# Optimization experiments

Hardware: AMD Instinct MI355X
Metric: run time of the kernel (lower is better)

Reference implementation:

```python
import jax, jax.numpy as jnp
import numpy as np
import math

H = 8
D_MODEL = 512
D_K = D_MODEL // H
NEG = -1.0e9


def setup_inputs() -> dict:
    key = jax.random.key(0)
    ks = jax.random.split(key, 10)
    B, S, D = 8, 1024, D_MODEL
    s = 1.0 / math.sqrt(D)
    return {
        "query": jax.random.normal(ks[0], (B, S, D), jnp.float32),
        "key": jax.random.normal(ks[1], (B, S, D), jnp.float32),
        "value": jax.random.normal(ks[2], (B, S, D), jnp.float32),
        "group_prob": jax.random.uniform(ks[3], (B, S, S), jnp.float32),
        "Wq": jax.random.normal(ks[4], (D, D), jnp.float32) * s,
        "Wk": jax.random.normal(ks[5], (D, D), jnp.float32) * s,
        "Wv": jax.random.normal(ks[6], (D, D), jnp.float32) * s,
        "Wh": jax.random.normal(ks[7], (D, D), jnp.float32) * s,
        "bh": jax.random.normal(ks[8], (D,), jnp.float32) * s,
        "mask": jax.random.randint(ks[9], (B, S, S), 0, 2, jnp.int32),
    }


def reference(query, key, value, group_prob, Wq, Wk, Wv, Wh, bh, mask):
    B, S, D = query.shape
    # project and split heads: [B, H, S, d_k]
    def split(x, W):
        return (x @ W.T).reshape(B, S, H, D_K).transpose(0, 2, 1, 3)
    q, k, v = split(query, Wq), split(key, Wk), split(value, Wv)
    scores = jnp.einsum('bhqd,bhkd->bhqk', q, k) / jnp.sqrt(jnp.asarray(D_K, q.dtype))
    # masked_fill where (mask | eye) == 0, i.e. keep mask-allowed or diagonal positions
    eye = jnp.eye(S, dtype=jnp.int32)
    allowed = (mask[:, None, :, :] | eye[None, None, :, :]) != 0  # [B,1,S,S]
    scores = jnp.where(allowed, scores, jnp.asarray(NEG, scores.dtype))
    p_attn = jax.nn.softmax(scores, axis=-1)
    p_attn = p_attn * group_prob[:, None, :, :]  # post-softmax group scaling
    x = jnp.einsum('bhqk,bhkd->bhqd', p_attn, v)
    x = x.transpose(0, 2, 1, 3).reshape(B, S, D)
    return x @ Wh.T + bh
```

## Files before the change

### kernel.cpp

```cpp
#include <hip/hip_runtime.h>
#include <hip/hip_bf16.h>
#include <cstdint>


typedef __attribute__((ext_vector_type(8))) short short8;
typedef __attribute__((ext_vector_type(4))) float f32x4;

__device__ __forceinline__ ushort f2bf(float x) {
    union { __hip_bfloat16 h; ushort u; } v;
    v.h = __float2bfloat16(x);
    return v.u;
}
__device__ __forceinline__ float bf2f(ushort u) {
    union { uint u; float f; } v; v.u = ((uint)u) << 16; return v.f;
}
__device__ __forceinline__ uint cvtpk(float lo, float hi) {
    uint r;
    asm("v_cvt_pk_bf16_f32 %0, %1, %2" : "=v"(r) : "v"(lo), "v"(hi));
    return r;
}
__device__ __forceinline__ f32x4 mfma16(short8 a, short8 b, f32x4 c) {
    return __builtin_amdgcn_mfma_f32_16x16x32_bf16(a, b, c, 0, 0, 0);
}
__device__ __forceinline__ void gl16(const void* g, const void* l) {
    __builtin_amdgcn_global_load_lds(
        (const __attribute__((address_space(1))) uint32_t*)(uintptr_t)g,
        (__attribute__((address_space(3))) uint32_t*)(uint32_t)(uintptr_t)l,
        16, 0, 0);
}

__global__ __launch_bounds__(256)
void prep(const float* __restrict__ q, const float* __restrict__ k,
          const float* __restrict__ v,
          const float* __restrict__ wq, const float* __restrict__ wk,
          const float* __restrict__ wv, const float* __restrict__ wh,
          const int* __restrict__ mask, const float* __restrict__ gp,
          ushort* __restrict__ qb, ushort* __restrict__ kb,
          ushort* __restrict__ vb,
          ushort* __restrict__ wqb, ushort* __restrict__ wkb,
          ushort* __restrict__ wvb, ushort* __restrict__ whb,
          ushort* __restrict__ gmb)
{
    const int bid = blockIdx.x, tid = threadIdx.x;
    if (bid < 8192) {
        size_t i = ((size_t)bid * 256 + tid) * 4;
        int4 m = *(const int4*)(mask + i);
        float4 gg = *(const float4*)(gp + i);
        int kk = (int)(i & 1023), qq = (int)((i >> 10) & 1023);
        uint u01 = cvtpk(gg.x, gg.y), u23 = cvtpk(gg.z, gg.w);
        ushort4 o;
        o.x = (m.x != 0 || qq == kk + 0) ? (ushort)(u01 & 0xffff) : (ushort)0xBF80;
        o.y = (m.y != 0 || qq == kk + 1) ? (ushort)(u01 >> 16)    : (ushort)0xBF80;
        o.z = (m.z != 0 || qq == kk + 2) ? (ushort)(u23 & 0xffff) : (ushort)0xBF80;
        o.w = (m.w != 0 || qq == kk + 3) ? (ushort)(u23 >> 16)    : (ushort)0xBF80;
        *(ushort4*)(gmb + i) = o;
    } else if (bid < 20480) {
        size_t id = ((size_t)(bid - 8192) * 256 + tid) * 4;
        int t = (int)(id >> 22);
        size_t off = id & 4194303;
        const float* s = (t == 0) ? q : (t == 1) ? k : v;
        ushort* d = (t == 0) ? qb : (t == 1) ? kb : vb;
        float4 x = *(const float4*)(s + off);
        uint2 o; o.x = cvtpk(x.x, x.y); o.y = cvtpk(x.z, x.w);
        *(uint2*)(d + off) = o;
    } else {
        size_t id = ((size_t)(bid - 20480) * 256 + tid) * 4;
        int t = (int)(id >> 18);
        size_t off = id & 262143;
        const float* s = (t == 0) ? wq : (t == 1) ? wk : (t == 2) ? wv : wh;
        ushort* d = (t == 0) ? wqb : (t == 1) ? wkb : (t == 2) ? wvb : whb;
        float4 x = *(const float4*)(s + off);
        uint2 o; o.x = cvtpk(x.x, x.y); o.y = cvtpk(x.z, x.w);
        *(uint2*)(d + off) = o;
    }
}

__global__ __launch_bounds__(256, 2)
void gemm3(const ushort* __restrict__ qb, const ushort* __restrict__ kb,
           const ushort* __restrict__ vb,
           const ushort* __restrict__ Wqb, const ushort* __restrict__ Wkb,
           const ushort* __restrict__ Wvb,
           ushort* __restrict__ q_ws, ushort* __restrict__ k_ws,
           ushort* __restrict__ vT)
{
    __shared__ __attribute__((aligned(16))) ushort As[8192];
    __shared__ __attribute__((aligned(16))) ushort Bs[8192];

    const int z = blockIdx.z;
    const ushort* A = (z == 0) ? qb : (z == 1) ? kb : Wvb;
    const ushort* B = (z == 0) ? Wqb : (z == 1) ? Wkb : vb;
    const int mt = (z == 2) ? blockIdx.y : blockIdx.x;
    const int nt = (z == 2) ? blockIdx.x : blockIdx.y;
    const int m0 = mt * 128, n0 = nt * 128;
    const int tid = threadIdx.x, lane = tid & 63, wave = tid >> 6;
    const int l15 = lane & 15, g = lane >> 4;
    const int wm = wave >> 1, wn = wave & 1;

    const int cb = (lane & 7) << 4;
    int soff[4];
    #pragma unroll
    for (int it = 0; it < 4; ++it) {
        int r = (it * 4 + wave) * 8 + (lane >> 3);
        soff[it] = r * 1024 + (cb ^ ((r & 7) << 4));
    }
    const char* Ab = (const char*)A + (size_t)m0 * 1024;
    const char* Bb = (const char*)B + (size_t)n0 * 1024;

    const int sw = (l15 & 7) << 4;
    const int c0 = (g * 16) ^ sw;
    const int c1 = (64 + g * 16) ^ sw;

    f32x4 acc[4][4];
    #pragma unroll
    for (int i = 0; i < 4; ++i)
        #pragma unroll
        for (int j = 0; j < 4; ++j) acc[i][j] = (f32x4){0.f, 0.f, 0.f, 0.f};

    for (int ks = 0; ks < 8; ++ks) {
        const int kof = ks * 128;
        #pragma unroll
        for (int it = 0; it < 4; ++it) {
            gl16(Ab + soff[it] + kof, (const char*)As + (it * 4 + wave) * 1024);
            gl16(Bb + soff[it] + kof, (const char*)Bs + (it * 4 + wave) * 1024);
        }
        __syncthreads();
        #pragma unroll
        for (int kk = 0; kk < 2; ++kk) {
            const int cc = kk ? c1 : c0;
            short8 af[4], bf[4];
            #pragma unroll
            for (int i = 0; i < 4; ++i)
                af[i] = *(const short8*)((const char*)As + (wm * 64 + i * 16 + l15) * 128 + cc);
            #pragma unroll
            for (int j = 0; j < 4; ++j)
                bf[j] = *(const short8*)((const char*)Bs + (wn * 64 + j * 16 + l15) * 128 + cc);
            #pragma unroll
            for (int i = 0; i < 4; ++i)
                #pragma unroll
                for (int j = 0; j < 4; ++j)
                    acc[i][j] = mfma16(af[i], bf[j], acc[i][j]);
        }
        __syncthreads();
    }

    #pragma unroll
    for (int i = 0; i < 4; ++i) {
        #pragma unroll
        for (int j = 0; j < 4; ++j) {
            #pragma unroll
            for (int r = 0; r < 4; ++r) {
                int mm = m0 + wm * 64 + i * 16 + g * 4 + r;
                int nn = n0 + wn * 64 + j * 16 + l15;
                float val = acc[i][j][r];
                if (z == 0) {
                    val *= 0.18033688f;
                    int b = mm >> 10, s = mm & 1023, h = nn >> 6, dk = nn & 63;
                    q_ws[((((size_t)(b * 8 + h)) << 10) + s) * 64 + dk] = f2bf(val);
                } else if (z == 1) {
                    int b = mm >> 10, s = mm & 1023, h = nn >> 6, dk = nn & 63;
                    k_ws[((((size_t)(b * 8 + h)) << 10) + s) * 64 + dk] = f2bf(val);
                } else {
                    int h = mm >> 6, d = mm & 63, b = nn >> 10, s = nn & 1023;
                    vT[(((size_t)(b * 8 + h) * 64 + d) << 10) + s] = f2bf(val);
                }
            }
        }
    }
}

__global__ __launch_bounds__(256, 2)
void gemm_o(const ushort* __restrict__ Xh, const ushort* __restrict__ Whb,
            const float* __restrict__ bias, float* __restrict__ out)
{
    __shared__ __attribute__((aligned(16))) ushort As[8192];
    __shared__ __attribute__((aligned(16))) ushort Bs[8192];

    const int m0 = blockIdx.x * 128, n0 = blockIdx.y * 128;
    const int tid = threadIdx.x, lane = tid & 63, wave = tid >> 6;
    const int l15 = lane & 15, g = lane >> 4;
    const int wm = wave >> 1, wn = wave & 1;
    const int bb = m0 >> 10, s0 = m0 & 1023;

    const int cb = (lane & 7) << 4;
    int aoff[4], boff[4];
    #pragma unroll
    for (int it = 0; it < 4; ++it) {
        int r = (it * 4 + wave) * 8 + (lane >> 3);
        int swz = cb ^ ((r & 7) << 4);
        aoff[it] = ((bb * 8) * 1024 + s0 + r) * 128 + swz;
        boff[it] = (n0 + r) * 1024 + swz;
    }
    const int sw = (l15 & 7) << 4;
    const int c0 = (g * 16) ^ sw;
    const int c1 = (64 + g * 16) ^ sw;

    f32x4 acc[4][4];
    #pragma unroll
    for (int i = 0; i < 4; ++i)
        #pragma unroll
        for (int j = 0; j < 4; ++j) acc[i][j] = (f32x4){0.f, 0.f, 0.f, 0.f};

    for (int ks = 0; ks < 8; ++ks) {
        #pragma unroll
        for (int it = 0; it < 4; ++it) {
            gl16((const char*)Xh + aoff[it] + ks * 131072,
                 (const char*)As + (it * 4 + wave) * 1024);
            gl16((const char*)Whb + boff[it] + ks * 128,
                 (const char*)Bs + (it * 4 + wave) * 1024);
        }
        __syncthreads();
        #pragma unroll
        for (int kk = 0; kk < 2; ++kk) {
            const int cc = kk ? c1 : c0;
            short8 af[4], bf[4];
            #pragma unroll
            for (int i = 0; i < 4; ++i)
                af[i] = *(const short8*)((const char*)As + (wm * 64 + i * 16 + l15) * 128 + cc);
            #pragma unroll
            for (int j = 0; j < 4; ++j)
                bf[j] = *(const short8*)((const char*)Bs + (wn * 64 + j * 16 + l15) * 128 + cc);
            #pragma unroll
            for (int i = 0; i < 4; ++i)
                #pragma unroll
                for (int j = 0; j < 4; ++j)
                    acc[i][j] = mfma16(af[i], bf[j], acc[i][j]);
        }
        __syncthreads();
    }

    float bv[4];
    #pragma unroll
    for (int j = 0; j < 4; ++j) bv[j] = bias[n0 + wn * 64 + j * 16 + l15];

    #pragma unroll
    for (int i = 0; i < 4; ++i)
        #pragma unroll
        for (int j = 0; j < 4; ++j)
            #pragma unroll
            for (int r = 0; r < 4; ++r) {
                int mm = m0 + wm * 64 + i * 16 + g * 4 + r;
                int nn = n0 + wn * 64 + j * 16 + l15;
                out[(size_t)mm * 512 + nn] = acc[i][j][r] + bv[j];
            }
}

__global__ __launch_bounds__(256, 4)
void attn(const ushort* __restrict__ Qh, const ushort* __restrict__ Kh,
          const ushort* __restrict__ Vt, const ushort* __restrict__ gm,
          ushort* __restrict__ xo)
{
    __shared__ __attribute__((aligned(16))) ushort kv[2][2][4096];

    const int w = blockIdx.x;
    const int bh = w & 63, qt = w >> 6;
    const int tid = threadIdx.x, wave = tid >> 6, lane = tid & 63;
    const int l15 = lane & 15, g = lane >> 4;
    const int q0 = qt * 64 + wave * 16;
    const int b = bh >> 3;

    const char* Kpb = (const char*)(Kh + (size_t)bh * 65536);
    const char* Vpb = (const char*)(Vt + (size_t)bh * 65536);
    const ushort* Qp = Qh + ((size_t)bh * 1024 + q0 + l15) * 64;
    const ushort* gmp = gm + ((size_t)b * 1024 + q0 + l15) * 1024;

    const short8 qf0 = *(const short8*)(Qp + g * 8);
    const short8 qf1 = *(const short8*)(Qp + 32 + g * 8);

    const int cb = (lane & 7) << 4;
    const int rA = wave * 8 + (lane >> 3);
    const int rB = rA + 32;
    const int gkA = (rA & 3) + 4 * ((rA >> 4) & 1) + 8 * ((rA >> 2) & 3) + 32 * (rA >> 5);
    const int gkB = (rB & 3) + 4 * ((rB >> 4) & 1) + 8 * ((rB >> 2) & 3) + 32 * (rB >> 5);
    const int okA = gkA * 128 + (cb ^ ((rA & 7) << 4));
    const int okB = gkB * 128 + (cb ^ ((rB & 7) << 4));
    const int ovA = rA * 2048 + (cb ^ ((rA & 7) << 4));
    const int ovB = rB * 2048 + (cb ^ ((rB & 7) << 4));

    const int sw = (l15 & 7) << 4;
    const int c0 = (g * 16) ^ sw;
    const int c1 = (64 + g * 16) ^ sw;

    f32x4 ot[4];
    #pragma unroll
    for (int t = 0; t < 4; ++t) ot[t] = (f32x4){0.f, 0.f, 0.f, 0.f};
    float m2 = -1.0e30f, lsum = 0.f;

    gl16(Kpb + okA, &kv[0][0][wave * 512]);
    gl16(Kpb + okB, &kv[0][0][(4 + wave) * 512]);
    gl16(Vpb + ovA, &kv[0][1][wave * 512]);
    gl16(Vpb + ovB, &kv[0][1][(4 + wave) * 512]);
    short8 gmc0 = *(const short8*)(gmp + g * 8);
    short8 gmc1 = *(const short8*)(gmp + 32 + g * 8);
    __syncthreads();

    for (int t = 0; t < 16; ++t) {
        const int cur = t & 1;
        short8 gmn0, gmn1;
        if (t < 15) {
            const char* kp = Kpb + (size_t)(t + 1) * 8192;
            const char* vp = Vpb + (size_t)(t + 1) * 128;
            gl16(kp + okA, &kv[cur ^ 1][0][wave * 512]);
            gl16(kp + okB, &kv[cur ^ 1][0][(4 + wave) * 512]);
            gl16(vp + ovA, &kv[cur ^ 1][1][wave * 512]);
            gl16(vp + ovB, &kv[cur ^ 1][1][(4 + wave) * 512]);
            gmn0 = *(const short8*)(gmp + (t + 1) * 64 + g * 8);
            gmn1 = *(const short8*)(gmp + (t + 1) * 64 + 32 + g * 8);
        }
        const char* kbuf = (const char*)&kv[cur][0][0];
        const char* vbuf = (const char*)&kv[cur][1][0];

        f32x4 s4[4];
        #pragma unroll
        for (int t4 = 0; t4 < 4; ++t4) {
            const char* ka = kbuf + (t4 * 16 + l15) * 128;
            short8 k0f = *(const short8*)(ka + c0);
            short8 k1f = *(const short8*)(ka + c1);
            f32x4 zz = (f32x4){0.f, 0.f, 0.f, 0.f};
            zz = mfma16(k0f, qf0, zz);
            zz = mfma16(k1f, qf1, zz);
            s4[t4] = zz;
        }

        float gv[16], svv[16];
        #pragma unroll
        for (int c = 0; c < 2; ++c) {
            const short8 gc = c ? gmc1 : gmc0;
            #pragma unroll
            for (int j = 0; j < 8; ++j) {
                const int jj = c * 8 + j;
                const int t4 = 2 * c + (j >> 2), r = j & 3;
                float gvv = bf2f((ushort)gc[j]);
                gv[jj] = gvv;
                svv[jj] = (gvv >= 0.f) ? s4[t4][r] : -1.0e9f;
            }
        }
        float x0 = fmaxf(fmaxf(svv[0], svv[1]), fmaxf(svv[2], svv[3]));
        float x1 = fmaxf(fmaxf(svv[4], svv[5]), fmaxf(svv[6], svv[7]));
        float x2 = fmaxf(fmaxf(svv[8], svv[9]), fmaxf(svv[10], svv[11]));
        float x3 = fmaxf(fmaxf(svv[12], svv[13]), fmaxf(svv[14], svv[15]));
        float tmax = fmaxf(fmaxf(x0, x1), fmaxf(x2, x3));
        tmax = fmaxf(tmax, __shfl_xor(tmax, 16, 64));
        tmax = fmaxf(tmax, __shfl_xor(tmax, 32, 64));

        if (__any(tmax > m2 + 4.0f)) {
            float mnew = fmaxf(m2, tmax);
            float corr = exp2f(m2 - mnew);
            m2 = mnew; lsum *= corr;
            #pragma unroll
            for (int t4 = 0; t4 < 4; ++t4) {
                ot[t4][0] *= corr; ot[t4][1] *= corr;
                ot[t4][2] *= corr; ot[t4][3] *= corr;
            }
        }

        float p[16];
        #pragma unroll
        for (int jj = 0; jj < 16; ++jj) p[jj] = exp2f(svv[jj] - m2);
        lsum += (((p[0] + p[1]) + (p[2] + p[3])) + ((p[4] + p[5]) + (p[6] + p[7])))
              + (((p[8] + p[9]) + (p[10] + p[11])) + ((p[12] + p[13]) + (p[14] + p[15])));
        union { uint4 u; short8 s; } pa0, pa1;
        pa0.u.x = cvtpk(p[0] * gv[0],  p[1] * gv[1]);
        pa0.u.y = cvtpk(p[2] * gv[2],  p[3] * gv[3]);
        pa0.u.z = cvtpk(p[4] * gv[4],  p[5] * gv[5]);
        pa0.u.w = cvtpk(p[6] * gv[6],  p[7] * gv[7]);
        pa1.u.x = cvtpk(p[8] * gv[8],  p[9] * gv[9]);
        pa1.u.y = cvtpk(p[10] * gv[10], p[11] * gv[11]);
        pa1.u.z = cvtpk(p[12] * gv[12], p[13] * gv[13]);
        pa1.u.w = cvtpk(p[14] * gv[14], p[15] * gv[15]);

        #pragma unroll
        for (int td = 0; td < 4; ++td) {
            const char* va = vbuf + (td * 16 + l15) * 128;
            short8 v0 = *(const short8*)(va + c0);
            short8 v1 = *(const short8*)(va + c1);
            ot[td] = mfma16(v0, pa0.s, ot[td]);
            ot[td] = mfma16(v1, pa1.s, ot[td]);
        }
        __syncthreads();
        if (t < 15) { gmc0 = gmn0; gmc1 = gmn1; }
    }

    lsum += __shfl_xor(lsum, 16, 64);
    lsum += __shfl_xor(lsum, 32, 64);
    const float inv = 1.0f / lsum;

    ushort* xp = xo + ((size_t)bh * 1024 + q0 + l15) * 64;
    #pragma unroll
    for (int td = 0; td < 4; ++td) {
        uint2 o;
        o.x = cvtpk(ot[td][0] * inv, ot[td][1] * inv);
        o.y = cvtpk(ot[td][2] * inv, ot[td][3] * inv);
        *(uint2*)(xp + td * 16 + g * 4) = o;
    }
}

extern "C" void kernel_launch(void* const* d_in, const int* in_sizes, int n_in,
                              void* d_out, int out_size, void* d_ws, size_t ws_size,
                              hipStream_t stream)
{
    const float* query = (const float*)d_in[0];
    const float* key   = (const float*)d_in[1];
    const float* value = (const float*)d_in[2];
    const float* gprob = (const float*)d_in[3];
    const float* Wq    = (const float*)d_in[4];
    const float* Wk    = (const float*)d_in[5];
    const float* Wv    = (const float*)d_in[6];
    const float* Wh    = (const float*)d_in[7];
    const float* bh    = (const float*)d_in[8];
    const int*   mask  = (const int*)d_in[9];
    float* out = (float*)d_out;

    ushort* ws = (ushort*)d_ws;
    const size_t HS = (size_t)64 * 65536;
    ushort* q_ws = ws;
    ushort* k_ws = ws + HS;
    ushort* vT   = ws + 2 * HS;
    ushort* gmb  = ws + 3 * HS;
    ushort* qb   = ws + 5 * HS;
    ushort* kb   = ws + 6 * HS;
    ushort* vb   = ws + 7 * HS;
    ushort* wqb  = ws + 8 * HS;
    ushort* wkb  = wqb + 262144;
    ushort* wvb  = wkb + 262144;
    ushort* whb  = wvb + 262144;
    ushort* x_ws = qb;

    prep<<<21504, 256, 0, stream>>>(query, key, value, Wq, Wk, Wv, Wh,
                                    mask, gprob, qb, kb, vb,
                                    wqb, wkb, wvb, whb, gmb);
    gemm3<<<dim3(64, 4, 3), 256, 0, stream>>>(qb, kb, vb, wqb, wkb, wvb,
                                              q_ws, k_ws, vT);
    attn<<<1024, 256, 0, stream>>>(q_ws, k_ws, vT, gmb, x_ws);
    gemm_o<<<dim3(64, 4), 256, 0, stream>>>(x_ws, whb, bh, out);
}
```

Measured before the change: 102.3 us.

## Process two query tiles per wave and drop online softmax max tracking

Each wave in the attention kernel now handles 32 query rows as two 16-row tiles. Every K/V fragment read from LDS feeds twice as many MFMAs, and the block count drops to 512. The running-max rescaling in the softmax is removed: exponentials are taken directly on the raw scores and normalised at the end, which removes the cross-lane max reduction and the rescale branch. In exchange it doubles accumulator and score registers (launch bounds relaxed to 2 blocks per SIMD group), halves the grid, and risks overflow if scores ever become large.

```diff
diff --git a/kernel.cpp b/kernel.cpp
--- a/kernel.cpp
+++ b/kernel.cpp
@@ -244,7 +244,7 @@
             }
 }
 
-__global__ __launch_bounds__(256, 4)
+__global__ __launch_bounds__(256, 2)
 void attn(const ushort* __restrict__ Qh, const ushort* __restrict__ Kh,
           const ushort* __restrict__ Vt, const ushort* __restrict__ gm,
           ushort* __restrict__ xo)
@@ -255,16 +255,20 @@
     const int bh = w & 63, qt = w >> 6;
     const int tid = threadIdx.x, wave = tid >> 6, lane = tid & 63;
     const int l15 = lane & 15, g = lane >> 4;
-    const int q0 = qt * 64 + wave * 16;
+    const int q0 = qt * 128 + wave * 32;
     const int b = bh >> 3;
 
     const char* Kpb = (const char*)(Kh + (size_t)bh * 65536);
     const char* Vpb = (const char*)(Vt + (size_t)bh * 65536);
-    const ushort* Qp = Qh + ((size_t)bh * 1024 + q0 + l15) * 64;
-    const ushort* gmp = gm + ((size_t)b * 1024 + q0 + l15) * 1024;
-
-    const short8 qf0 = *(const short8*)(Qp + g * 8);
-    const short8 qf1 = *(const short8*)(Qp + 32 + g * 8);
+    const ushort* QpA = Qh + ((size_t)bh * 1024 + q0 + l15) * 64;
+    const ushort* QpB = QpA + 16 * 64;
+    const ushort* gmpA = gm + ((size_t)b * 1024 + q0 + l15) * 1024;
+    const ushort* gmpB = gmpA + 16 * 1024;
+
+    const short8 qa0 = *(const short8*)(QpA + g * 8);
+    const short8 qa1 = *(const short8*)(QpA + 32 + g * 8);
+    const short8 qb0 = *(const short8*)(QpB + g * 8);
+    const short8 qb1 = *(const short8*)(QpB + 32 + g * 8);
 
     const int cb = (lane & 7) << 4;
     const int rA = wave * 8 + (lane >> 3);
@@ -280,22 +284,27 @@
     const int c0 = (g * 16) ^ sw;
     const int c1 = (64 + g * 16) ^ sw;
 
-    f32x4 ot[4];
-    #pragma unroll
-    for (int t = 0; t < 4; ++t) ot[t] = (f32x4){0.f, 0.f, 0.f, 0.f};
-    float m2 = -1.0e30f, lsum = 0.f;
+    f32x4 otA[4], otB[4];
+    #pragma unroll
+    for (int t = 0; t < 4; ++t) {
+        otA[t] = (f32x4){0.f, 0.f, 0.f, 0.f};
+        otB[t] = (f32x4){0.f, 0.f, 0.f, 0.f};
+    }
+    float lsA = 0.f, lsB = 0.f;
 
     gl16(Kpb + okA, &kv[0][0][wave * 512]);
     gl16(Kpb + okB, &kv[0][0][(4 + wave) * 512]);
     gl16(Vpb + ovA, &kv[0][1][wave * 512]);
     gl16(Vpb + ovB, &kv[0][1][(4 + wave) * 512]);
-    short8 gmc0 = *(const short8*)(gmp + g * 8);
-    short8 gmc1 = *(const short8*)(gmp + 32 + g * 8);
+    short8 gcA0 = *(const short8*)(gmpA + g * 8);
+    short8 gcA1 = *(const short8*)(gmpA + 32 + g * 8);
+    short8 gcB0 = *(const short8*)(gmpB + g * 8);
+    short8 gcB1 = *(const short8*)(gmpB + 32 + g * 8);
     __syncthreads();
 
     for (int t = 0; t < 16; ++t) {
         const int cur = t & 1;
-        short8 gmn0, gmn1;
+        short8 gnA0, gnA1, gnB0, gnB1;
         if (t < 15) {
             const char* kp = Kpb + (size_t)(t + 1) * 8192;
             const char* vp = Vpb + (size_t)(t + 1) * 128;
@@ -303,94 +312,114 @@
             gl16(kp + okB, &kv[cur ^ 1][0][(4 + wave) * 512]);
             gl16(vp + ovA, &kv[cur ^ 1][1][wave * 512]);
             gl16(vp + ovB, &kv[cur ^ 1][1][(4 + wave) * 512]);
-            gmn0 = *(const short8*)(gmp + (t + 1) * 64 + g * 8);
-            gmn1 = *(const short8*)(gmp + (t + 1) * 64 + 32 + g * 8);
+            gnA0 = *(const short8*)(gmpA + (t + 1) * 64 + g * 8);
+            gnA1 = *(const short8*)(gmpA + (t + 1) * 64 + 32 + g * 8);
+            gnB0 = *(const short8*)(gmpB + (t + 1) * 64 + g * 8);
+            gnB1 = *(const short8*)(gmpB + (t + 1) * 64 + 32 + g * 8);
         }
         const char* kbuf = (const char*)&kv[cur][0][0];
         const char* vbuf = (const char*)&kv[cur][1][0];
 
-        f32x4 s4[4];
+        f32x4 sA[4], sB[4];
         #pragma unroll
         for (int t4 = 0; t4 < 4; ++t4) {
             const char* ka = kbuf + (t4 * 16 + l15) * 128;
             short8 k0f = *(const short8*)(ka + c0);
             short8 k1f = *(const short8*)(ka + c1);
-            f32x4 zz = (f32x4){0.f, 0.f, 0.f, 0.f};
-            zz = mfma16(k0f, qf0, zz);
-            zz = mfma16(k1f, qf1, zz);
-            s4[t4] = zz;
-        }
-
-        float gv[16], svv[16];
-        #pragma unroll
-        for (int c = 0; c < 2; ++c) {
-            const short8 gc = c ? gmc1 : gmc0;
-            #pragma unroll
-            for (int j = 0; j < 8; ++j) {
-                const int jj = c * 8 + j;
-                const int t4 = 2 * c + (j >> 2), r = j & 3;
-                float gvv = bf2f((ushort)gc[j]);
-                gv[jj] = gvv;
-                svv[jj] = (gvv >= 0.f) ? s4[t4][r] : -1.0e9f;
+            f32x4 za = (f32x4){0.f, 0.f, 0.f, 0.f};
+            za = mfma16(k0f, qa0, za);
+            za = mfma16(k1f, qa1, za);
+            sA[t4] = za;
+            f32x4 zb = (f32x4){0.f, 0.f, 0.f, 0.f};
+            zb = mfma16(k0f, qb0, zb);
+            zb = mfma16(k1f, qb1, zb);
+            sB[t4] = zb;
+        }
+
+        union { uint4 u; short8 s; } paA0, paA1, paB0, paB1;
+        {
+            float p[16], gv[16];
+            #pragma unroll
+            for (int c = 0; c < 2; ++c) {
+                const short8 gc = c ? gcA1 : gcA0;
+                #pragma unroll
+                for (int j = 0; j < 8; ++j) {
+                    const int jj = c * 8 + j;
+                    const int t4 = 2 * c + (j >> 2), r = j & 3;
+                    float gvv = bf2f((ushort)gc[j]);
+                    gv[jj] = gvv;
+                    p[jj] = exp2f((gvv >= 0.f) ? sA[t4][r] : -1.0e9f);
+                }
             }
-        }
-        float x0 = fmaxf(fmaxf(svv[0], svv[1]), fmaxf(svv[2], svv[3]));
-        float x1 = fmaxf(fmaxf(svv[4], svv[5]), fmaxf(svv[6], svv[7]));
-        float x2 = fmaxf(fmaxf(svv[8], svv[9]), fmaxf(svv[10], svv[11]));
-        float x3 = fmaxf(fmaxf(svv[12], svv[13]), fmaxf(svv[14], svv[15]));
-        float tmax = fmaxf(fmaxf(x0, x1), fmaxf(x2, x3));
-        tmax = fmaxf(tmax, __shfl_xor(tmax, 16, 64));
-        tmax = fmaxf(tmax, __shfl_xor(tmax, 32, 64));
-
-        if (__any(tmax > m2 + 4.0f)) {
-            float mnew = fmaxf(m2, tmax);
-            float corr = exp2f(m2 - mnew);
-            m2 = mnew; lsum *= corr;
-            #pragma unroll
-            for (int t4 = 0; t4 < 4; ++t4) {
-                ot[t4][0] *= corr; ot[t4][1] *= corr;
-                ot[t4][2] *= corr; ot[t4][3] *= corr;
+            lsA += (((p[0] + p[1]) + (p[2] + p[3])) + ((p[4] + p[5]) + (p[6] + p[7])))
+                 + (((p[8] + p[9]) + (p[10] + p[11])) + ((p[12] + p[13]) + (p[14] + p[15])));
+            paA0.u.x = cvtpk(p[0] * gv[0],  p[1] * gv[1]);
+            paA0.u.y = cvtpk(p[2] * gv[2],  p[3] * gv[3]);
+            paA0.u.z = cvtpk(p[4] * gv[4],  p[5] * gv[5]);
+            paA0.u.w = cvtpk(p[6] * gv[6],  p[7] * gv[7]);
+            paA1.u.x = cvtpk(p[8] * gv[8],  p[9] * gv[9]);
+            paA1.u.y = cvtpk(p[10] * gv[10], p[11] * gv[11]);
+            paA1.u.z = cvtpk(p[12] * gv[12], p[13] * gv[13]);
+            paA1.u.w = cvtpk(p[14] * gv[14], p[15] * gv[15]);
+        }
+        {
+            float p[16], gv[16];
+            #pragma unroll
+            for (int c = 0; c < 2; ++c) {
+                const short8 gc = c ? gcB1 : gcB0;
+                #pragma unroll
+                for (int j = 0; j < 8; ++j) {
+                    const int jj = c * 8 + j;
+                    const int t4 = 2 * c + (j >> 2), r = j & 3;
+                    float gvv = bf2f((ushort)gc[j]);
+                    gv[jj] = gvv;
+                    p[jj] = exp2f((gvv >= 0.f) ? sB[t4][r] : -1.0e9f);
+                }
             }
-        }
-
-        float p[16];
-        #pragma unroll
-        for (int jj = 0; jj < 16; ++jj) p[jj] = exp2f(svv[jj] - m2);
-        lsum += (((p[0] + p[1]) + (p[2] + p[3])) + ((p[4] + p[5]) + (p[6] + p[7])))
-              + (((p[8] + p[9]) + (p[10] + p[11])) + ((p[12] + p[13]) + (p[14] + p[15])));
-        union { uint4 u; short8 s; } pa0, pa1;
-        pa0.u.x = cvtpk(p[0] * gv[0],  p[1] * gv[1]);
-        pa0.u.y = cvtpk(p[2] * gv[2],  p[3] * gv[3]);
-        pa0.u.z = cvtpk(p[4] * gv[4],  p[5] * gv[5]);
-        pa0.u.w = cvtpk(p[6] * gv[6],  p[7] * gv[7]);
-        pa1.u.x = cvtpk(p[8] * gv[8],  p[9] * gv[9]);
-        pa1.u.y = cvtpk(p[10] * gv[10], p[11] * gv[11]);
-        pa1.u.z = cvtpk(p[12] * gv[12], p[13] * gv[13]);
-        pa1.u.w = cvtpk(p[14] * gv[14], p[15] * gv[15]);
+            lsB += (((p[0] + p[1]) + (p[2] + p[3])) + ((p[4] + p[5]) + (p[6] + p[7])))
+                 + (((p[8] + p[9]) + (p[10] + p[11])) + ((p[12] + p[13]) + (p[14] + p[15])));
+            paB0.u.x = cvtpk(p[0] * gv[0],  p[1] * gv[1]);
+            paB0.u.y = cvtpk(p[2] * gv[2],  p[3] * gv[3]);
+            paB0.u.z = cvtpk(p[4] * gv[4],  p[5] * gv[5]);
+            paB0.u.w = cvtpk(p[6] * gv[6],  p[7] * gv[7]);
+            paB1.u.x = cvtpk(p[8] * gv[8],  p[9] * gv[9]);
+            paB1.u.y = cvtpk(p[10] * gv[10], p[11] * gv[11]);
+            paB1.u.z = cvtpk(p[12] * gv[12], p[13] * gv[13]);
+            paB1.u.w = cvtpk(p[14] * gv[14], p[15] * gv[15]);
+        }
 
         #pragma unroll
         for (int td = 0; td < 4; ++td) {
             const char* va = vbuf + (td * 16 + l15) * 128;
             short8 v0 = *(const short8*)(va + c0);
             short8 v1 = *(const short8*)(va + c1);
-            ot[td] = mfma16(v0, pa0.s, ot[td]);
-            ot[td] = mfma16(v1, pa1.s, ot[td]);
+            otA[td] = mfma16(v0, paA0.s, otA[td]);
+            otA[td] = mfma16(v1, paA1.s, otA[td]);
+            otB[td] = mfma16(v0, paB0.s, otB[td]);
+            otB[td] = mfma16(v1, paB1.s, otB[td]);
         }
         __syncthreads();
-        if (t < 15) { gmc0 = gmn0; gmc1 = gmn1; }
-    }
-
-    lsum += __shfl_xor(lsum, 16, 64);
-    lsum += __shfl_xor(lsum, 32, 64);
-    const float inv = 1.0f / lsum;
-
-    ushort* xp = xo + ((size_t)bh * 1024 + q0 + l15) * 64;
+        if (t < 15) { gcA0 = gnA0; gcA1 = gnA1; gcB0 = gnB0; gcB1 = gnB1; }
+    }
+
+    lsA += __shfl_xor(lsA, 16, 64);
+    lsA += __shfl_xor(lsA, 32, 64);
+    lsB += __shfl_xor(lsB, 16, 64);
+    lsB += __shfl_xor(lsB, 32, 64);
+    const float invA = 1.0f / lsA;
+    const float invB = 1.0f / lsB;
+
+    ushort* xpA = xo + ((size_t)bh * 1024 + q0 + l15) * 64;
+    ushort* xpB = xpA + 16 * 64;
     #pragma unroll
     for (int td = 0; td < 4; ++td) {
-        uint2 o;
-        o.x = cvtpk(ot[td][0] * inv, ot[td][1] * inv);
-        o.y = cvtpk(ot[td][2] * inv, ot[td][3] * inv);
-        *(uint2*)(xp + td * 16 + g * 4) = o;
+        uint2 oa, ob;
+        oa.x = cvtpk(otA[td][0] * invA, otA[td][1] * invA);
+        oa.y = cvtpk(otA[td][2] * invA, otA[td][3] * invA);
+        ob.x = cvtpk(otB[td][0] * invB, otB[td][1] * invB);
+        ob.y = cvtpk(otB[td][2] * invB, otB[td][3] * invB);
+        *(uint2*)(xpA + td * 16 + g * 4) = oa;
+        *(uint2*)(xpB + td * 16 + g * 4) = ob;
     }
 }
 
@@ -430,6 +459,6 @@
                                     wqb, wkb, wvb, whb, gmb);
     gemm3<<<dim3(64, 4, 3), 256, 0, stream>>>(qb, kb, vb, wqb, wkb, wvb,
                                               q_ws, k_ws, vT);
-    attn<<<1024, 256, 0, stream>>>(q_ws, k_ws, vT, gmb, x_ws);
+    attn<<<512, 256, 0, stream>>>(q_ws, k_ws, vT, gmb, x_ws);
     gemm_o<<<dim3(64, 4), 256, 0, stream>>>(x_ws, whb, bh, out);
 }
```

After: 101.8 us (median of 2 runs). No clear change (-0.5%).
